# Kernel optimization log

Measured on AMD Instinct MI355X. Metric: run time of the kernel, lower is better.

## Reference

```python
import jax, jax.numpy as jnp
import numpy as np


def _avgpool(x, k):
    # x: [B, C, H, W] -> [B, C, H//k, W//k] via non-overlapping mean pooling
    B, C, H, W = x.shape
    return x.reshape(B, C, H // k, k, W // k, k).mean(axis=(3, 5))


def _multiscale_tokens(x):
    # concat flattened pooled maps along token dim: [B, C, sum_k (H/k)*(W/k)]
    B, C, H, W = x.shape
    parts = [_avgpool(x, k).reshape(B, C, -1) for k in (16, 8, 4, 2)]
    return jnp.concatenate(parts, axis=2)


def setup_inputs() -> dict:
    key = jax.random.key(0)
    x = jax.random.normal(key, (16, 256, 128, 128), dtype=jnp.float32)
    gamma = jnp.zeros((1,), dtype=jnp.float32)
    return {"x": x, "gamma": gamma}


def reference(x, gamma):
    B, C, H, W = x.shape
    # q and k pooling are identical in the original module (recomputed redundantly)
    tokens = _multiscale_tokens(x)                      # [B, C, T]
    energy = jnp.einsum('bct,bdt->bcd', tokens, tokens)  # [B, C, C]
    energy_new = jnp.max(energy, axis=-1, keepdims=True) - energy
    attention = jax.nn.softmax(energy_new, axis=-1)      # [B, C, C]
    proj_value = x.reshape(B, C, H * W)                  # [B, C, HW]
    out = jnp.einsum('bcd,bdn->bcn', attention, proj_value).reshape(B, C, H, W)
    return gamma * out + x
```

## Files before the change

### kernel.cpp

```cpp
#include <hip/hip_runtime.h>
#include <hip/hip_bf16.h>

#define B_  16
#define C_  256
#define W_  128
#define HW_ 16384
#define T_  5440
#define NSPLIT 10

typedef __bf16 bf16;
typedef __bf16 bf16x2 __attribute__((ext_vector_type(2)));
typedef __bf16 bf16x4 __attribute__((ext_vector_type(4)));
typedef __bf16 bf16x8 __attribute__((ext_vector_type(8)));
typedef float  f32x4  __attribute__((ext_vector_type(4)));

__device__ __forceinline__ void gload_lds16(const void* g, void* l) {
    __builtin_amdgcn_global_load_lds(
        (const __attribute__((address_space(1))) void*)g,
        (__attribute__((address_space(3))) void*)l, 16, 0, 0);
}

__device__ __forceinline__ int bs64(int n, int q) {
    return (n & 3) * 1024 + q * 256 + (((n >> 2) ^ (q << 1)) & 15) * 16;
}

__global__ __launch_bounds__(256) void pool_kernel(const float* __restrict__ x,
                                                   bf16* __restrict__ tokens) {
    __shared__ float s2[64 * 64];
    __shared__ float s4[32 * 32];
    __shared__ float s8[16 * 16];
    const int blk = blockIdx.x;
    const float* plane = x + ((size_t)blk << 14);
    bf16* tok = tokens + (size_t)blk * T_;
    const int tid = threadIdx.x;

    for (int it = 0; it < 8; ++it) {
        int task = it * 256 + tid;
        int i  = task >> 5;
        int jp = task & 31;
        const float4 r0 = *(const float4*)(plane + (2 * i) * W_ + 4 * jp);
        const float4 r1 = *(const float4*)(plane + (2 * i + 1) * W_ + 4 * jp);
        float p0 = (r0.x + r0.y + r1.x + r1.y) * 0.25f;
        float p1 = (r0.z + r0.w + r1.z + r1.w) * 0.25f;
        s2[i * 64 + 2 * jp]     = p0;
        s2[i * 64 + 2 * jp + 1] = p1;
        bf16x2 wv; wv.x = (bf16)p0; wv.y = (bf16)p1;
        *(bf16x2*)(tok + 1344 + i * 64 + 2 * jp) = wv;
    }
    __syncthreads();
    for (int it = 0; it < 4; ++it) {
        int task = it * 256 + tid;
        int i = task >> 5, j = task & 31;
        float v = 0.25f * (s2[(2 * i) * 64 + 2 * j] + s2[(2 * i) * 64 + 2 * j + 1] +
                           s2[(2 * i + 1) * 64 + 2 * j] + s2[(2 * i + 1) * 64 + 2 * j + 1]);
        s4[i * 32 + j] = v;
        tok[320 + i * 32 + j] = (bf16)v;
    }
    __syncthreads();
    {
        int i = tid >> 4, j = tid & 15;
        float v = 0.25f * (s4[(2 * i) * 32 + 2 * j] + s4[(2 * i) * 32 + 2 * j + 1] +
                           s4[(2 * i + 1) * 32 + 2 * j] + s4[(2 * i + 1) * 32 + 2 * j + 1]);
        s8[i * 16 + j] = v;
        tok[64 + tid] = (bf16)v;
    }
    __syncthreads();
    if (tid < 64) {
        int i = tid >> 3, j = tid & 7;
        float v = 0.25f * (s8[(2 * i) * 16 + 2 * j] + s8[(2 * i) * 16 + 2 * j + 1] +
                           s8[(2 * i + 1) * 16 + 2 * j] + s8[(2 * i + 1) * 16 + 2 * j + 1]);
        tok[tid] = (bf16)v;
    }
}

__global__ __launch_bounds__(256, 2) void energy_kernel(const bf16* __restrict__ tokens,
                                                        float* __restrict__ part) {
    __shared__ __align__(16) char smem[32768];
    const int blk  = blockIdx.x;
    const int s    = blk / 48;
    const int rem  = blk - s * 48;
    const int b    = rem / 3;
    const int tile = rem - b * 3;
    const int cm0  = (tile == 2) ? 128 : 0;
    const int cn0  = (tile == 0) ? 0 : 128;
    const bool offdiag = (tile == 1);
    const int kbase = s * (T_ / NSPLIT);
    const int tid  = threadIdx.x;
    const int lane = tid & 63;
    const int w    = tid >> 6;
    const int wm = (w >> 1) * 64, wn = (w & 1) * 64;
    const int lm = lane & 15;
    const int q8 = (lane >> 4) * 8;
    const bf16* tokb = tokens + (size_t)b * C_ * T_;

    #define E_STAGE(ki, d) do {                                                   \
        const int k0_ = kbase + (ki) * 32;                                        \
        _Pragma("unroll")                                                         \
        for (int it = 0; it < 2; ++it) {                                          \
            int slot = it * 256 + tid;                                            \
            int r  = slot >> 2;                                                   \
            int c8 = (slot & 3) * 8;                                              \
            gload_lds16(tokb + (size_t)(cm0 + r) * T_ + k0_ + c8,                 \
                        smem + (size_t)(d) * 8192 + (size_t)(it * 256 + w * 64) * 16); \
        }                                                                         \
        if (offdiag) {                                                            \
            _Pragma("unroll")                                                     \
            for (int it = 0; it < 2; ++it) {                                      \
                int slot = it * 256 + tid;                                        \
                int r  = slot >> 2;                                               \
                int c8 = (slot & 3) * 8;                                          \
                gload_lds16(tokb + (size_t)(cn0 + r) * T_ + k0_ + c8,             \
                            smem + 16384 + (size_t)(d) * 8192 + (size_t)(it * 256 + w * 64) * 16); \
            }                                                                     \
        }                                                                         \
    } while (0)

    f32x4 acc[4][4] = {};
    E_STAGE(0, 0);
    __syncthreads();
    for (int ki = 0; ki < 17; ++ki) {
        if (ki < 16) E_STAGE(ki + 1, (ki + 1) & 1);
        const bf16* Af = (const bf16*)(smem + (ki & 1) * 8192);
        const bf16* Bf = offdiag ? (const bf16*)(smem + 16384 + (ki & 1) * 8192) : Af;
        bf16x8 af[4], bfr[4];
        #pragma unroll
        for (int mi = 0; mi < 4; ++mi)
            af[mi] = *(const bf16x8*)(Af + (wm + mi * 16 + lm) * 32 + q8);
        #pragma unroll
        for (int ni = 0; ni < 4; ++ni)
            bfr[ni] = *(const bf16x8*)(Bf + (wn + ni * 16 + lm) * 32 + q8);
        #pragma unroll
        for (int mi = 0; mi < 4; ++mi)
            #pragma unroll
            for (int ni = 0; ni < 4; ++ni)
                acc[mi][ni] = __builtin_amdgcn_mfma_f32_16x16x32_bf16(af[mi], bfr[ni], acc[mi][ni], 0, 0, 0);
        __syncthreads();
    }
    #undef E_STAGE
    float* P = part + ((size_t)(s * 4096 + b * C_) << 8);
    const int row0 = (lane >> 4) * 4;
    for (int mi = 0; mi < 4; ++mi)
        for (int ni = 0; ni < 4; ++ni) {
            f32x4 v = acc[mi][ni];
            int row = cm0 + wm + mi * 16 + row0;
            int col = cn0 + wn + ni * 16 + lm;
            #pragma unroll
            for (int e = 0; e < 4; ++e)
                P[((size_t)(row + e) << 8) + col] = v[e];
            if (offdiag)
                *(f32x4*)(P + ((size_t)col << 8) + row) = v;
        }
}

__global__ __launch_bounds__(256) void softmax_kernel(const float* __restrict__ part,
                                                      bf16* __restrict__ att) {
    const int row  = blockIdx.x * 4 + (threadIdx.x >> 6);
    const int lane = threadIdx.x & 63;
    float4 e = {0.f, 0.f, 0.f, 0.f};
    for (int s = 0; s < NSPLIT; ++s) {
        const float4 p = *(const float4*)(part + ((size_t)(s * 4096 + row) << 8) + lane * 4);
        e.x += p.x; e.y += p.y; e.z += p.z; e.w += p.w;
    }
    float mn = fminf(fminf(e.x, e.y), fminf(e.z, e.w));
    for (int off = 32; off > 0; off >>= 1) mn = fminf(mn, __shfl_xor(mn, off));
    float p0 = __expf(mn - e.x), p1 = __expf(mn - e.y);
    float p2 = __expf(mn - e.z), p3 = __expf(mn - e.w);
    float s = p0 + p1 + p2 + p3;
    for (int off = 32; off > 0; off >>= 1) s += __shfl_xor(s, off);
    float inv = 1.0f / s;
    bf16x4 o;
    o.x = (bf16)(p0 * inv); o.y = (bf16)(p1 * inv);
    o.z = (bf16)(p2 * inv); o.w = (bf16)(p3 * inv);
    *(bf16x4*)(att + ((size_t)row << 8) + lane * 4) = o;
}

__global__ __launch_bounds__(512, 2) void out_kernel(const bf16* __restrict__ att,
                                                     const float* __restrict__ x,
                                                     const float* __restrict__ gamma,
                                                     float* __restrict__ out) {
    __shared__ __align__(16) char smem[106496];
    float* Vf = (float*)smem;
    const int b  = blockIdx.x >> 8;
    const int n0 = (blockIdx.x & 255) << 6;
    const int tid  = threadIdx.x;
    const int lane = tid & 63;
    const int w    = tid >> 6;
    const int wm   = w * 32;
    const int lm = lane & 15;
    const int q4 = lane >> 4;
    const int q8 = q4 * 8;
    const float g = gamma[0];
    const bf16*  attb = att + ((size_t)b << 16);
    const float* xb   = x + ((size_t)b << 22);
    const int gn = tid & 15;
    const int kp = tid >> 4;
    const bool vthread = (tid < 256);

    #define A_STAGE(kk, d) do {                                                   \
        const int k0_ = (kk) * 32;                                                \
        _Pragma("unroll")                                                         \
        for (int it = 0; it < 2; ++it) {                                          \
            int slot = it * 512 + tid;                                            \
            int r  = slot >> 2;                                                   \
            int c8 = (slot & 3) * 8;                                              \
            gload_lds16(attb + ((size_t)r << 8) + k0_ + c8,                       \
                        smem + 65536 + (size_t)(d) * 16384 + (size_t)(it * 512 + w * 64) * 16); \
        }                                                                         \
    } while (0)

    f32x4 acc[2][4] = {};
    f32x4 vj0, vj1;

    if (vthread) {
        vj0 = *(const f32x4*)(xb + ((size_t)(2 * kp) << 14) + n0 + gn * 4);
        vj1 = *(const f32x4*)(xb + ((size_t)(2 * kp + 1) << 14) + n0 + gn * 4);
        *(f32x4*)(Vf + (2 * kp) * 64 + gn * 4)     = vj0;
        *(f32x4*)(Vf + (2 * kp + 1) * 64 + gn * 4) = vj1;
        char* Bs0 = smem + 98304;
        #pragma unroll
        for (int e = 0; e < 4; ++e) {
            bf16x2 wv; wv.x = (bf16)vj0[e]; wv.y = (bf16)vj1[e];
            *(bf16x2*)(Bs0 + bs64(gn * 4 + e, kp >> 2) + 4 * (kp & 3)) = wv;
        }
    }
    A_STAGE(0, 0);
    __syncthreads();

    for (int kk = 0; kk < 8; ++kk) {
        if (kk < 7) {
            if (vthread) {
                const float* xs = xb + ((size_t)((kk + 1) * 32 + 2 * kp) << 14) + n0 + gn * 4;
                vj0 = *(const f32x4*)(xs);
                vj1 = *(const f32x4*)(xs + HW_);
            }
            A_STAGE(kk + 1, (kk + 1) & 1);
        }
        const bf16* Af  = (const bf16*)(smem + 65536 + (kk & 1) * 16384);
        const char* BsR = smem + 98304 + (kk & 1) * 4096;
        bf16x8 af[2];
        #pragma unroll
        for (int mi = 0; mi < 2; ++mi)
            af[mi] = *(const bf16x8*)(Af + (wm + mi * 16 + lm) * 32 + q8);
        #pragma unroll
        for (int ni = 0; ni < 4; ++ni) {
            bf16x8 bb = *(const bf16x8*)(BsR + bs64(ni * 16 + lm, q4));
            #pragma unroll
            for (int mi = 0; mi < 2; ++mi)
                acc[mi][ni] = __builtin_amdgcn_mfma_f32_16x16x32_bf16(af[mi], bb, acc[mi][ni], 0, 0, 0);
        }
        if (kk < 7 && vthread) {
            const int c0 = (kk + 1) * 32 + 2 * kp;
            *(f32x4*)(Vf + (c0)     * 64 + gn * 4) = vj0;
            *(f32x4*)(Vf + (c0 + 1) * 64 + gn * 4) = vj1;
            char* BsW = smem + 98304 + ((kk + 1) & 1) * 4096;
            #pragma unroll
            for (int e = 0; e < 4; ++e) {
                bf16x2 wv; wv.x = (bf16)vj0[e]; wv.y = (bf16)vj1[e];
                *(bf16x2*)(BsW + bs64(gn * 4 + e, kp >> 2) + 4 * (kp & 3)) = wv;
            }
        }
        __syncthreads();
    }
    #undef A_STAGE

    float* buf = (float*)(smem + 65536) + w * 1024;
    for (int mi = 0; mi < 2; ++mi) {
        #pragma unroll
        for (int ni = 0; ni < 4; ++ni) {
            f32x4 v = acc[mi][ni];
            int c = ni * 16 + lm;
            buf[(q4 * 4 + 0) * 64 + c] = v[0];
            buf[(q4 * 4 + 1) * 64 + c] = v[1];
            buf[(q4 * 4 + 2) * 64 + c] = v[2];
            buf[(q4 * 4 + 3) * 64 + c] = v[3];
        }
        #pragma unroll
        for (int it = 0; it < 4; ++it) {
            int idx = it * 64 + lane;
            int r  = idx >> 4;
            int c4 = (idx & 15) * 4;
            f32x4 pv = *(const f32x4*)(buf + r * 64 + c4);
            int c = wm + mi * 16 + r;
            f32x4 xv = *(const f32x4*)(Vf + c * 64 + c4);
            f32x4 o;
            o[0] = g * pv[0] + xv[0];
            o[1] = g * pv[1] + xv[1];
            o[2] = g * pv[2] + xv[2];
            o[3] = g * pv[3] + xv[3];
            size_t gi = ((size_t)b << 22) + ((size_t)c << 14) + n0 + c4;
            __builtin_nontemporal_store(o, (f32x4*)(out + gi));
        }
    }
}

__global__ __launch_bounds__(256) void fallback_copy(const float* __restrict__ x,
                                                     const float* __restrict__ gamma,
                                                     float* __restrict__ out, size_t n) {
    size_t i = (size_t)blockIdx.x * 256 + threadIdx.x;
    size_t stride = (size_t)gridDim.x * 256;
    float g = gamma[0];
    for (; i < n; i += stride) out[i] = x[i] + g * 0.0f;
}

extern "C" void kernel_launch(void* const* d_in, const int* in_sizes, int n_in,
                              void* d_out, int out_size, void* d_ws, size_t ws_size,
                              hipStream_t stream) {
    const float* x     = (const float*)d_in[0];
    const float* gamma = (const float*)d_in[1];
    float* out = (float*)d_out;

    const size_t ATT_BYTES = (size_t)B_ * C_ * C_ * 2;
    if (ws_size < ATT_BYTES) {
        size_t n = (size_t)B_ * C_ * HW_;
        fallback_copy<<<2048, 256, 0, stream>>>(x, gamma, out, n);
        return;
    }
    bf16*  tokens = (bf16*)d_out;
    float* part   = (float*)((char*)d_out + ((size_t)64 << 20));
    bf16*  att    = (bf16*)d_ws;

    pool_kernel<<<dim3(B_ * C_), dim3(256), 0, stream>>>(x, tokens);
    energy_kernel<<<dim3(NSPLIT * B_ * 3), dim3(256), 0, stream>>>(tokens, part);
    softmax_kernel<<<dim3(B_ * C_ / 4), dim3(256), 0, stream>>>(part, att);
    out_kernel<<<dim3(B_ * 256), dim3(512), 0, stream>>>(att, x, gamma, out);
}
```

Baseline: 579.9 us.

## Shrink out_kernel tile to 32 columns, drop fp32 V staging in LDS

Restructures the output GEMM kernel to use 256-thread blocks over 32-column tiles, twice as many blocks, with each wave covering 64 rows by 32 columns. The fp32 copy of x is no longer kept in shared memory; the residual add re-reads x from global memory in the epilogue. This cuts LDS use from about 104KB to 36KB per block so more blocks fit per CU. The cost is a second global read of x, which may be served by cache, plus narrower tiles and scalar bf16 LDS writes for the B operand.

```diff
diff --git a/kernel.cpp b/kernel.cpp
--- a/kernel.cpp
+++ b/kernel.cpp
@@ -20,8 +20,8 @@
         (__attribute__((address_space(3))) void*)l, 16, 0, 0);
 }
 
-__device__ __forceinline__ int bs64(int n, int q) {
-    return (n & 3) * 1024 + q * 256 + (((n >> 2) ^ (q << 1)) & 15) * 16;
+__device__ __forceinline__ int bs32(int n, int q) {
+    return (n & 3) * 512 + q * 128 + (((n >> 2) ^ (q << 1)) & 7) * 16;
 }
 
 __global__ __launch_bounds__(256) void pool_kernel(const float* __restrict__ x,
@@ -174,120 +174,106 @@
     *(bf16x4*)(att + ((size_t)row << 8) + lane * 4) = o;
 }
 
-__global__ __launch_bounds__(512, 2) void out_kernel(const bf16* __restrict__ att,
+__global__ __launch_bounds__(256, 4) void out_kernel(const bf16* __restrict__ att,
                                                      const float* __restrict__ x,
                                                      const float* __restrict__ gamma,
                                                      float* __restrict__ out) {
-    __shared__ __align__(16) char smem[106496];
-    float* Vf = (float*)smem;
-    const int b  = blockIdx.x >> 8;
-    const int n0 = (blockIdx.x & 255) << 6;
+    __shared__ __align__(16) char smem[36864];
+    const int b  = blockIdx.x >> 9;
+    const int n0 = (blockIdx.x & 511) << 5;
     const int tid  = threadIdx.x;
     const int lane = tid & 63;
     const int w    = tid >> 6;
-    const int wm   = w * 32;
+    const int wm   = w * 64;
     const int lm = lane & 15;
     const int q4 = lane >> 4;
     const int q8 = q4 * 8;
     const float g = gamma[0];
     const bf16*  attb = att + ((size_t)b << 16);
     const float* xb   = x + ((size_t)b << 22);
-    const int gn = tid & 15;
-    const int kp = tid >> 4;
-    const bool vthread = (tid < 256);
-
-    #define A_STAGE(kk, d) do {                                                   \
-        const int k0_ = (kk) * 32;                                                \
-        _Pragma("unroll")                                                         \
-        for (int it = 0; it < 2; ++it) {                                          \
-            int slot = it * 512 + tid;                                            \
-            int r  = slot >> 2;                                                   \
-            int c8 = (slot & 3) * 8;                                              \
-            gload_lds16(attb + ((size_t)r << 8) + k0_ + c8,                       \
-                        smem + 65536 + (size_t)(d) * 16384 + (size_t)(it * 512 + w * 64) * 16); \
-        }                                                                         \
+    const int vk = tid >> 3;
+    const int vj = tid & 7;
+    const int vq = vk >> 3;
+    const int vh = (vk & 7) * 2;
+
+    #define A_STAGE(kk, d) do {                                                  \
+        const int k0_ = (kk) * 32;                                               \
+        _Pragma("unroll")                                                        \
+        for (int it = 0; it < 4; ++it) {                                         \
+            int slot = it * 256 + tid;                                           \
+            int r  = slot >> 2;                                                  \
+            int c8 = (slot & 3) * 8;                                             \
+            gload_lds16(attb + ((size_t)r << 8) + k0_ + c8,                      \
+                        smem + (size_t)(d) * 16384 + (size_t)(it * 256 + w * 64) * 16); \
+        }                                                                        \
     } while (0)
 
-    f32x4 acc[2][4] = {};
-    f32x4 vj0, vj1;
-
-    if (vthread) {
-        vj0 = *(const f32x4*)(xb + ((size_t)(2 * kp) << 14) + n0 + gn * 4);
-        vj1 = *(const f32x4*)(xb + ((size_t)(2 * kp + 1) << 14) + n0 + gn * 4);
-        *(f32x4*)(Vf + (2 * kp) * 64 + gn * 4)     = vj0;
-        *(f32x4*)(Vf + (2 * kp + 1) * 64 + gn * 4) = vj1;
-        char* Bs0 = smem + 98304;
-        #pragma unroll
-        for (int e = 0; e < 4; ++e) {
-            bf16x2 wv; wv.x = (bf16)vj0[e]; wv.y = (bf16)vj1[e];
-            *(bf16x2*)(Bs0 + bs64(gn * 4 + e, kp >> 2) + 4 * (kp & 3)) = wv;
-        }
-    }
+    #define BS_WRITE(d, v) do {                                                  \
+        char* BsW = smem + 32768 + (size_t)(d) * 2048;                           \
+        _Pragma("unroll")                                                        \
+        for (int e = 0; e < 4; ++e) {                                            \
+            bf16 hv = (bf16)(v)[e];                                              \
+            *(bf16*)(BsW + bs32(vj * 4 + e, vq) + vh) = hv;                      \
+        }                                                                        \
+    } while (0)
+
+    f32x4 acc[4][2] = {};
+    f32x4 vv;
+
+    vv = *(const f32x4*)(xb + ((size_t)vk << 14) + n0 + vj * 4);
+    BS_WRITE(0, vv);
     A_STAGE(0, 0);
     __syncthreads();
 
     for (int kk = 0; kk < 8; ++kk) {
         if (kk < 7) {
-            if (vthread) {
-                const float* xs = xb + ((size_t)((kk + 1) * 32 + 2 * kp) << 14) + n0 + gn * 4;
-                vj0 = *(const f32x4*)(xs);
-                vj1 = *(const f32x4*)(xs + HW_);
-            }
+            vv = *(const f32x4*)(xb + ((size_t)((kk + 1) * 32 + vk) << 14) + n0 + vj * 4);
             A_STAGE(kk + 1, (kk + 1) & 1);
         }
-        const bf16* Af  = (const bf16*)(smem + 65536 + (kk & 1) * 16384);
-        const char* BsR = smem + 98304 + (kk & 1) * 4096;
-        bf16x8 af[2];
-        #pragma unroll
-        for (int mi = 0; mi < 2; ++mi)
+        const bf16* Af  = (const bf16*)(smem + (kk & 1) * 16384);
+        const char* BsR = smem + 32768 + (kk & 1) * 2048;
+        bf16x8 af[4];
+        #pragma unroll
+        for (int mi = 0; mi < 4; ++mi)
             af[mi] = *(const bf16x8*)(Af + (wm + mi * 16 + lm) * 32 + q8);
         #pragma unroll
-        for (int ni = 0; ni < 4; ++ni) {
-            bf16x8 bb = *(const bf16x8*)(BsR + bs64(ni * 16 + lm, q4));
+        for (int ni = 0; ni < 2; ++ni) {
+            bf16x8 bb = *(const bf16x8*)(BsR + bs32(ni * 16 + lm, q4));
             #pragma unroll
-            for (int mi = 0; mi < 2; ++mi)
+            for (int mi = 0; mi < 4; ++mi)
                 acc[mi][ni] = __builtin_amdgcn_mfma_f32_16x16x32_bf16(af[mi], bb, acc[mi][ni], 0, 0, 0);
         }
-        if (kk < 7 && vthread) {
-            const int c0 = (kk + 1) * 32 + 2 * kp;
-            *(f32x4*)(Vf + (c0)     * 64 + gn * 4) = vj0;
-            *(f32x4*)(Vf + (c0 + 1) * 64 + gn * 4) = vj1;
-            char* BsW = smem + 98304 + ((kk + 1) & 1) * 4096;
-            #pragma unroll
-            for (int e = 0; e < 4; ++e) {
-                bf16x2 wv; wv.x = (bf16)vj0[e]; wv.y = (bf16)vj1[e];
-                *(bf16x2*)(BsW + bs64(gn * 4 + e, kp >> 2) + 4 * (kp & 3)) = wv;
-            }
-        }
+        if (kk < 7) BS_WRITE((kk + 1) & 1, vv);
         __syncthreads();
     }
     #undef A_STAGE
-
-    float* buf = (float*)(smem + 65536) + w * 1024;
-    for (int mi = 0; mi < 2; ++mi) {
-        #pragma unroll
-        for (int ni = 0; ni < 4; ++ni) {
+    #undef BS_WRITE
+
+    float* buf = (float*)(smem + (size_t)w * 2176);
+    for (int mi = 0; mi < 4; ++mi) {
+        #pragma unroll
+        for (int ni = 0; ni < 2; ++ni) {
             f32x4 v = acc[mi][ni];
             int c = ni * 16 + lm;
-            buf[(q4 * 4 + 0) * 64 + c] = v[0];
-            buf[(q4 * 4 + 1) * 64 + c] = v[1];
-            buf[(q4 * 4 + 2) * 64 + c] = v[2];
-            buf[(q4 * 4 + 3) * 64 + c] = v[3];
-        }
-        #pragma unroll
-        for (int it = 0; it < 4; ++it) {
+            buf[(q4 * 4 + 0) * 33 + c] = v[0];
+            buf[(q4 * 4 + 1) * 33 + c] = v[1];
+            buf[(q4 * 4 + 2) * 33 + c] = v[2];
+            buf[(q4 * 4 + 3) * 33 + c] = v[3];
+        }
+        #pragma unroll
+        for (int it = 0; it < 2; ++it) {
             int idx = it * 64 + lane;
-            int r  = idx >> 4;
-            int c4 = (idx & 15) * 4;
-            f32x4 pv = *(const f32x4*)(buf + r * 64 + c4);
+            int r  = idx >> 3;
+            int c4 = (idx & 7) * 4;
+            f32x4 pv = *(const f32x4*)(buf + r * 33 + c4);
             int c = wm + mi * 16 + r;
-            f32x4 xv = *(const f32x4*)(Vf + c * 64 + c4);
+            size_t gi = ((size_t)b << 22) + ((size_t)c << 14) + n0 + c4;
+            f32x4 xv = *(const f32x4*)(x + gi);
             f32x4 o;
             o[0] = g * pv[0] + xv[0];
             o[1] = g * pv[1] + xv[1];
             o[2] = g * pv[2] + xv[2];
             o[3] = g * pv[3] + xv[3];
-            size_t gi = ((size_t)b << 22) + ((size_t)c << 14) + n0 + c4;
             __builtin_nontemporal_store(o, (f32x4*)(out + gi));
         }
     }
@@ -322,5 +308,5 @@
     pool_kernel<<<dim3(B_ * C_), dim3(256), 0, stream>>>(x, tokens);
     energy_kernel<<<dim3(NSPLIT * B_ * 3), dim3(256), 0, stream>>>(tokens, part);
     softmax_kernel<<<dim3(B_ * C_ / 4), dim3(256), 0, stream>>>(part, att);
-    out_kernel<<<dim3(B_ * 256), dim3(512), 0, stream>>>(att, x, gamma, out);
-}
+    out_kernel<<<dim3(B_ * 512), dim3(256), 0, stream>>>(att, x, gamma, out);
+}
```

Measured after the change: 593.6 us. +2.4%, slower.
